# Optimization experiments

Measured on AMD Instinct MI355X. Metric: run time of the kernel, lower is better.

The kernel has to match this reference:

```python
import jax, jax.numpy as jnp
import numpy as np

EPS = 1e-5
N_HEAD = 8
D_MODEL = 1024
D_K = D_MODEL // N_HEAD


def setup_inputs() -> dict:
    key = jax.random.key(0)
    ks = jax.random.split(key, 6)
    B, N = 4, 8192
    scale = 0.02
    return {
        "query": jax.random.normal(ks[0], (B, N, D_MODEL), jnp.float32),
        "key": jax.random.normal(ks[1], (B, N, D_MODEL), jnp.float32),
        "value": jax.random.normal(ks[2], (B, N, D_MODEL), jnp.float32),
        "Wq": jax.random.normal(ks[3], (D_MODEL, D_MODEL), jnp.float32) * scale,
        "bq": jnp.zeros((D_MODEL,), jnp.float32),
        "Wk": jax.random.normal(ks[4], (D_MODEL, D_MODEL), jnp.float32) * scale,
        "bk": jnp.zeros((D_MODEL,), jnp.float32),
        "Wv": jax.random.normal(ks[5], (D_MODEL, D_MODEL), jnp.float32) * scale,
        "bv": jnp.zeros((D_MODEL,), jnp.float32),
        "gamma_K": jnp.ones((N_HEAD, D_K), jnp.float32),
        "beta_K": jnp.zeros((N_HEAD, D_K), jnp.float32),
        "gamma_V": jnp.ones((N_HEAD, D_K), jnp.float32),
        "beta_V": jnp.zeros((N_HEAD, D_K), jnp.float32),
    }


def _proj_heads(x, W, b):
    # x: [B,N,D], torch Linear: x @ W.T + b -> [B,H,N,d_k]
    B, N, _ = x.shape
    y = jnp.einsum('bnd,ed->bne', x, W) + b
    return y.reshape(B, N, N_HEAD, D_K).transpose(0, 2, 1, 3)


def _layernorm_per_head(x, gamma, beta):
    # x: [B,H,N,d_k]; gamma/beta: [H,d_k] broadcast over batch and seq
    mu = jnp.mean(x, axis=-1, keepdims=True)
    var = jnp.mean((x - mu) ** 2, axis=-1, keepdims=True)
    xn = (x - mu) * jax.lax.rsqrt(var + EPS)
    return xn * gamma[None, :, None, :] + beta[None, :, None, :]


def reference(query, key, value, Wq, bq, Wk, bk, Wv, bv,
              gamma_K, beta_K, gamma_V, beta_V):
    B, N, _ = query.shape
    q = _proj_heads(query, Wq, bq)   # [B,H,N,dk]
    k = _proj_heads(key, Wk, bk)
    v = _proj_heads(value, Wv, bv)
    # galerkin: layernorm on K and V per head
    k = _layernorm_per_head(k, gamma_K, beta_K)
    v = _layernorm_per_head(v, gamma_V, beta_V)
    # linear attention: (K^T V)/N then Q @ (.)
    scores = jnp.einsum('bhnd,bhne->bhde', k, v)  # [B,H,dk,dk]
    p_attn = scores / N
    x = jnp.einsum('bhnd,bhde->bhne', q, p_attn)  # [B,H,N,dk]
    att_output = x.transpose(0, 2, 1, 3).reshape(B, N, N_HEAD * D_K)
    return (att_output, p_attn)
```

## Files before the change

kernel.cpp:

```cpp
#include <hip/hip_runtime.h>
#include <stdint.h>

#define DM 1024
#define NHEAD 8
#define DK 128
#define BATCH 4
#define SEQ 8192
#define ROWS (BATCH*SEQ)
#define EPSL 1e-5f
#define NSPLIT 8

typedef __attribute__((ext_vector_type(8)))  short    bf16x8;
typedef __attribute__((ext_vector_type(4)))  short    short4v;
typedef __attribute__((ext_vector_type(4)))  float    f32x4;
typedef __attribute__((ext_vector_type(4)))  float    float4v;
typedef __attribute__((ext_vector_type(2)))  uint32_t uint2v;
typedef __attribute__((ext_vector_type(4)))  uint32_t uint4v;

union AFrag { bf16x8 v; short4v h[2]; int i4[4]; };
union U8    { uint4v v[2]; uint32_t u[8]; };

__device__ inline uint32_t pack2bf(float a, float b){
  uint32_t ua = __builtin_bit_cast(uint32_t, a) + 0x8000u;
  uint32_t ub = __builtin_bit_cast(uint32_t, b) + 0x8000u;
  return (ua >> 16) | (ub & 0xffff0000u);
}

__global__ void wconv_kernel(const float* __restrict__ src, uint32_t* __restrict__ dst, int n8){
  int i = blockIdx.x*256 + threadIdx.x;
  if (i >= n8) return;
  const float4v* s = (const float4v*)src;
  float4v v0 = s[2*i], v1 = s[2*i+1];
  uint4v o;
  o.x = pack2bf(v0.x, v0.y); o.y = pack2bf(v0.z, v0.w);
  o.z = pack2bf(v1.x, v1.y); o.w = pack2bf(v1.z, v1.w);
  ((uint4v*)dst)[i] = o;
}

template<int MODE>
__global__ __launch_bounds__(256, 2)
void gemm_core(const float* __restrict__ A, const uint16_t* __restrict__ Bw,
               const float* __restrict__ bias, const float* __restrict__ gamma,
               const float* __restrict__ beta, uint16_t* __restrict__ outb,
               float* __restrict__ outf)
{
  __shared__ uint16_t As[128][36];
  __shared__ uint16_t Bs[128][36];
  __shared__ float red_s[2][128];
  __shared__ float red_q[2][128];

  const int tid = threadIdx.x;
  const int bN = blockIdx.x, bM = blockIdx.y;
  const int lane = tid & 63, wv = tid >> 6;
  const int wm = wv & 1, wn = wv >> 1;
  const int l15 = lane & 15, l4 = lane >> 4;

  const int sr = tid >> 1, sh = tid & 1;
  const float* Ap = A + (size_t)(bM*128 + sr)*DM + sh*16;
  const uint16_t* Bbase = Bw + (MODE==1 ? (size_t)(bM>>6)*1048576 : (size_t)0);
  const uint16_t* Bp = Bbase + (size_t)(bN*128 + sr)*DM + sh*16;
  uint32_t* asw = (uint32_t*)&As[sr][sh*16];
  uint32_t* bsw = (uint32_t*)&Bs[sr][sh*16];

  f32x4 acc[4][4];
  #pragma unroll
  for (int i=0;i<4;i++)
    #pragma unroll
    for (int j=0;j<4;j++) acc[i][j] = (f32x4)(0.0f);

  const uint16_t* Ard = &As[wm*64 + l15][l4*8];
  const uint16_t* Brd = &Bs[wn*64 + l15][l4*8];

  for (int k0 = 0; k0 < DM; k0 += 32){
    float4v a0 = *(const float4v*)(Ap);
    float4v a1 = *(const float4v*)(Ap+4);
    float4v a2 = *(const float4v*)(Ap+8);
    float4v a3 = *(const float4v*)(Ap+12);
    uint4v b0 = *(const uint4v*)(Bp);
    uint4v b1 = *(const uint4v*)(Bp+8);
    Ap += 32; Bp += 32;
    uint32_t p0 = pack2bf(a0.x,a0.y), p1 = pack2bf(a0.z,a0.w);
    uint32_t p2 = pack2bf(a1.x,a1.y), p3 = pack2bf(a1.z,a1.w);
    uint32_t p4 = pack2bf(a2.x,a2.y), p5 = pack2bf(a2.z,a2.w);
    uint32_t p6 = pack2bf(a3.x,a3.y), p7 = pack2bf(a3.z,a3.w);
    __syncthreads();
    { uint2v t; t.x=p0;   t.y=p1;   ((uint2v*)asw)[0]=t; }
    { uint2v t; t.x=p2;   t.y=p3;   ((uint2v*)asw)[1]=t; }
    { uint2v t; t.x=p4;   t.y=p5;   ((uint2v*)asw)[2]=t; }
    { uint2v t; t.x=p6;   t.y=p7;   ((uint2v*)asw)[3]=t; }
    { uint2v t; t.x=b0.x; t.y=b0.y; ((uint2v*)bsw)[0]=t; }
    { uint2v t; t.x=b0.z; t.y=b0.w; ((uint2v*)bsw)[1]=t; }
    { uint2v t; t.x=b1.x; t.y=b1.y; ((uint2v*)bsw)[2]=t; }
    { uint2v t; t.x=b1.z; t.y=b1.w; ((uint2v*)bsw)[3]=t; }
    __syncthreads();

    AFrag af[4], bf4[4];
    #pragma unroll
    for (int mt=0; mt<4; mt++){
      af[mt].h[0] = *(const short4v*)(Ard + mt*16*36);
      af[mt].h[1] = *(const short4v*)(Ard + mt*16*36 + 4);
    }
    #pragma unroll
    for (int nt=0; nt<4; nt++){
      bf4[nt].h[0] = *(const short4v*)(Brd + nt*16*36);
      bf4[nt].h[1] = *(const short4v*)(Brd + nt*16*36 + 4);
    }
    #pragma unroll
    for (int mt=0; mt<4; mt++)
      #pragma unroll
      for (int nt=0; nt<4; nt++)
        acc[mt][nt] = __builtin_amdgcn_mfma_f32_16x16x32_bf16(af[mt].v, bf4[nt].v, acc[mt][nt], 0, 0, 0);
  }

  if (MODE == 0){
    float bv[4], gv[4], btv[4];
    #pragma unroll
    for (int nt=0; nt<4; nt++){
      int col = bN*128 + wn*64 + nt*16 + l15;
      bv[nt] = bias[col]; gv[nt] = gamma[col]; btv[nt] = beta[col];
    }
    #pragma unroll
    for (int mt=0; mt<4; mt++){
      #pragma unroll
      for (int i=0; i<4; i++){
        float sm = 0.f, sq = 0.f;
        #pragma unroll
        for (int nt=0; nt<4; nt++){
          float v = acc[mt][nt][i] + bv[nt];
          acc[mt][nt][i] = v;
          sm += v; sq += v*v;
        }
        #pragma unroll
        for (int off=1; off<16; off<<=1){
          sm += __shfl_xor(sm, off, 16);
          sq += __shfl_xor(sq, off, 16);
        }
        if (l15 == 0){
          int rl = wm*64 + mt*16 + l4*4 + i;
          red_s[wn][rl] = sm; red_q[wn][rl] = sq;
        }
      }
    }
    __syncthreads();
    #pragma unroll
    for (int mt=0; mt<4; mt++){
      #pragma unroll
      for (int i=0; i<4; i++){
        int rl = wm*64 + mt*16 + l4*4 + i;
        float sum = red_s[0][rl] + red_s[1][rl];
        float ssq = red_q[0][rl] + red_q[1][rl];
        float mean = sum * (1.f/DK);
        float var  = ssq * (1.f/DK) - mean*mean;
        float rs   = rsqrtf(var + EPSL);
        size_t row = (size_t)(bM*128 + rl);
        #pragma unroll
        for (int nt=0; nt<4; nt++){
          int col = bN*128 + wn*64 + nt*16 + l15;
          float o = (acc[mt][nt][i] - mean)*rs*gv[nt] + btv[nt];
          uint32_t u = __builtin_bit_cast(uint32_t, o) + 0x8000u;
          outb[row*DM + col] = (uint16_t)(u >> 16);
        }
      }
    }
  } else {
    const int bb = bM >> 6;
    float bv[4];
    #pragma unroll
    for (int nt=0; nt<4; nt++)
      bv[nt] = bias[bb*DM + bN*128 + wn*64 + nt*16 + l15];
    #pragma unroll
    for (int mt=0; mt<4; mt++){
      #pragma unroll
      for (int i=0; i<4; i++){
        size_t row = (size_t)(bM*128 + wm*64 + mt*16 + l4*4 + i);
        #pragma unroll
        for (int nt=0; nt<4; nt++){
          int col = bN*128 + wn*64 + nt*16 + l15;
          outf[row*DM + col] = acc[mt][nt][i] + bv[nt];
        }
      }
    }
  }
}

__global__ __launch_bounds__(256, 2)
void scores_kernel(const uint16_t* __restrict__ kln, const uint16_t* __restrict__ vln,
                   float* __restrict__ part)
{
  __shared__ uint16_t kT[128][70];
  __shared__ uint16_t vT[128][70];
  const int tid = threadIdx.x;
  const int sp = blockIdx.x & 7, bh = blockIdx.x >> 3;
  const int b = bh >> 3, h = bh & 7;
  const int lane = tid & 63, wv = tid >> 6, wm = wv & 1, wn = wv >> 1;
  const int l15 = lane & 15, l4 = lane >> 4;
  const int dg = tid & 7, np = tid >> 3;

  f32x4 acc[4][4];
  #pragma unroll
  for (int i=0;i<4;i++)
    #pragma unroll
    for (int j=0;j<4;j++) acc[i][j] = (f32x4)(0.0f);

  const size_t hb = (size_t)b*SEQ*DM + (size_t)h*DK;
  for (int nc = 0; nc < 16; nc++){
    const int n0 = sp*1024 + nc*64;
    const uint16_t* kp = kln + hb + (size_t)(n0 + 2*np)*DM + dg*16;
    const uint16_t* vp = vln + hb + (size_t)(n0 + 2*np)*DM + dg*16;
    U8 k0, k1, v0, v1;
    k0.v[0] = *(const uint4v*)(kp);       k0.v[1] = *(const uint4v*)(kp+8);
    k1.v[0] = *(const uint4v*)(kp+DM);    k1.v[1] = *(const uint4v*)(kp+DM+8);
    v0.v[0] = *(const uint4v*)(vp);       v0.v[1] = *(const uint4v*)(vp+8);
    v1.v[0] = *(const uint4v*)(vp+DM);    v1.v[1] = *(const uint4v*)(vp+DM+8);
    __syncthreads();
    #pragma unroll
    for (int q=0; q<8; q++){
      uint32_t ke = (k0.u[q] & 0xffffu) | (k1.u[q] << 16);
      uint32_t ko = (k0.u[q] >> 16)     | (k1.u[q] & 0xffff0000u);
      uint32_t ve = (v0.u[q] & 0xffffu) | (v1.u[q] << 16);
      uint32_t vo = (v0.u[q] >> 16)     | (v1.u[q] & 0xffff0000u);
      int d = dg*16 + q*2;
      *(uint32_t*)&kT[d  ][2*np] = ke;
      *(uint32_t*)&kT[d+1][2*np] = ko;
      *(uint32_t*)&vT[d  ][2*np] = ve;
      *(uint32_t*)&vT[d+1][2*np] = vo;
    }
    __syncthreads();
    #pragma unroll
    for (int ks=0; ks<2; ks++){
      const int koff = ks*32 + l4*8;
      AFrag af[4], bf4[4];
      #pragma unroll
      for (int mt=0; mt<4; mt++){
        const uint16_t* pr = &kT[wm*64 + mt*16 + l15][koff];
        af[mt].i4[0] = *(const int*)(pr);
        af[mt].i4[1] = *(const int*)(pr+2);
        af[mt].i4[2] = *(const int*)(pr+4);
        af[mt].i4[3] = *(const int*)(pr+6);
      }
      #pragma unroll
      for (int nt=0; nt<4; nt++){
        const uint16_t* pr = &vT[wn*64 + nt*16 + l15][koff];
        bf4[nt].i4[0] = *(const int*)(pr);
        bf4[nt].i4[1] = *(const int*)(pr+2);
        bf4[nt].i4[2] = *(const int*)(pr+4);
        bf4[nt].i4[3] = *(const int*)(pr+6);
      }
      #pragma unroll
      for (int mt=0; mt<4; mt++)
        #pragma unroll
        for (int nt=0; nt<4; nt++)
          acc[mt][nt] = __builtin_amdgcn_mfma_f32_16x16x32_bf16(af[mt].v, bf4[nt].v, acc[mt][nt], 0, 0, 0);
    }
  }
  float* po = part + (size_t)(sp*32 + bh)*16384;
  #pragma unroll
  for (int mt=0; mt<4; mt++)
    #pragma unroll
    for (int i=0; i<4; i++){
      int d = wm*64 + mt*16 + l4*4 + i;
      #pragma unroll
      for (int nt=0; nt<4; nt++){
        int e = wn*64 + nt*16 + l15;
        po[d*128 + e] = acc[mt][nt][i];
      }
    }
}

__global__ void reduce_kernel(const float* __restrict__ part, float* __restrict__ pout){
  int i = blockIdx.x*256 + threadIdx.x;
  const float4v* p4 = (const float4v*)part;
  float4v s = p4[i];
  #pragma unroll
  for (int sp2=1; sp2<NSPLIT; sp2++) s += p4[(size_t)sp2*131072 + i];
  s *= (1.0f/(float)SEQ);
  ((float4v*)pout)[i] = s;
}

__global__ __launch_bounds__(256)
void fold_kernel(const float* __restrict__ Wq, const float* __restrict__ p,
                 uint16_t* __restrict__ WcT)
{
  const int dblk = blockIdx.x, h = blockIdx.y, b = blockIdx.z;
  const int t = threadIdx.x;
  const int eg = t & 15, dq = t >> 4;
  const int e0 = eg*8, d0 = dq*8;
  const float* pbase = p + (size_t)((b*NHEAD + h)*DK)*DK;
  const float* wbase = Wq + (size_t)h*DK*DM + dblk*128;
  float accf[8][8];
  #pragma unroll
  for (int i=0;i<8;i++)
    #pragma unroll
    for (int j=0;j<8;j++) accf[i][j] = 0.f;
  for (int f=0; f<DK; f++){
    float4v pa = *(const float4v*)(pbase + f*DK + e0);
    float4v pc = *(const float4v*)(pbase + f*DK + e0 + 4);
    float4v wa = *(const float4v*)(wbase + (size_t)f*DM + d0);
    float4v wc = *(const float4v*)(wbase + (size_t)f*DM + d0 + 4);
    float pe[8] = {pa.x,pa.y,pa.z,pa.w,pc.x,pc.y,pc.z,pc.w};
    float we[8] = {wa.x,wa.y,wa.z,wa.w,wc.x,wc.y,wc.z,wc.w};
    #pragma unroll
    for (int i=0;i<8;i++)
      #pragma unroll
      for (int j=0;j<8;j++) accf[i][j] += pe[i]*we[j];
  }
  uint16_t* ob = WcT + (size_t)b*1048576 + (size_t)(h*DK)*DM + dblk*128;
  #pragma unroll
  for (int i=0;i<8;i++){
    uint4v ov;
    ov.x = pack2bf(accf[i][0], accf[i][1]);
    ov.y = pack2bf(accf[i][2], accf[i][3]);
    ov.z = pack2bf(accf[i][4], accf[i][5]);
    ov.w = pack2bf(accf[i][6], accf[i][7]);
    *(uint4v*)(ob + (size_t)(e0+i)*DM + d0) = ov;
  }
}

__global__ void bc_kernel(const float* __restrict__ bq, const float* __restrict__ p,
                          float* __restrict__ bc)
{
  int gid = blockIdx.x*256 + threadIdx.x;
  int b = gid >> 10, col = gid & 1023, h = col >> 7, e = col & 127;
  float s = 0.f;
  for (int f=0; f<DK; f++)
    s += bq[h*DK + f] * p[(size_t)((b*NHEAD + h)*DK + f)*DK + e];
  bc[gid] = s;
}

extern "C" void kernel_launch(void* const* d_in, const int* in_sizes, int n_in,
                              void* d_out, int out_size, void* d_ws, size_t ws_size,
                              hipStream_t stream)
{
  const float* query = (const float*)d_in[0];
  const float* key   = (const float*)d_in[1];
  const float* value = (const float*)d_in[2];
  const float* Wq    = (const float*)d_in[3];
  const float* bq    = (const float*)d_in[4];
  const float* Wk    = (const float*)d_in[5];
  const float* bk    = (const float*)d_in[6];
  const float* Wv    = (const float*)d_in[7];
  const float* bv    = (const float*)d_in[8];
  const float* gK    = (const float*)d_in[9];
  const float* bK    = (const float*)d_in[10];
  const float* gV    = (const float*)d_in[11];
  const float* bV    = (const float*)d_in[12];
  float* out = (float*)d_out;

  char* ws = (char*)d_ws;
  uint16_t* kln  = (uint16_t*)(ws);
  uint16_t* vln  = (uint16_t*)(ws + 67108864);
  uint16_t* wkb  = (uint16_t*)(ws + 134217728);
  uint16_t* wvb  = (uint16_t*)(ws + 136314880);
  float*    part = (float*)   (ws + 138412032);
  uint16_t* wct  = (uint16_t*)(ws + 155189248);
  float*    bc   = (float*)   (ws + 163577856);

  float* pout = out + 33554432;

  wconv_kernel<<<512, 256, 0, stream>>>(Wk, (uint32_t*)wkb, 131072);
  wconv_kernel<<<512, 256, 0, stream>>>(Wv, (uint32_t*)wvb, 131072);
  gemm_core<0><<<dim3(8,256), 256, 0, stream>>>(key,   wkb, bk, gK, bK, kln, nullptr);
  gemm_core<0><<<dim3(8,256), 256, 0, stream>>>(value, wvb, bv, gV, bV, vln, nullptr);
  scores_kernel<<<256, 256, 0, stream>>>(kln, vln, part);
  reduce_kernel<<<512, 256, 0, stream>>>(part, pout);
  fold_kernel<<<dim3(8,8,4), 256, 0, stream>>>(Wq, pout, wct);
  bc_kernel<<<16, 256, 0, stream>>>(bq, pout, bc);
  gemm_core<1><<<dim3(8,256), 256, 0, stream>>>(query, wct, bc, nullptr, nullptr, nullptr, out);
}
```

Baseline: 924.2 us.

## Prefetch next K-slab into registers and remap GEMM blocks across XCDs

The GEMM and scores kernels now issue the global loads for the next K (or sequence) slab right after the LDS write barrier, so memory latency overlaps the MFMA work on the current slab. The GEMM grid becomes 1D with an XCD-aware mapping: the 8 N-tiles of one M-row land on the same XCD, which is meant to improve L2 reuse of the A rows. The prefetch keeps more registers live, which could pressure occupancy under launch_bounds(256,2).

```diff
diff --git a/kernel.cpp b/kernel.cpp
--- a/kernel.cpp
+++ b/kernel.cpp
@@ -50,7 +50,10 @@
   __shared__ float red_q[2][128];
 
   const int tid = threadIdx.x;
-  const int bN = blockIdx.x, bM = blockIdx.y;
+  const int id  = blockIdx.x;
+  const int xcd = id & 7, j = id >> 3;
+  const int bM  = ((j >> 3) << 3) | xcd;
+  const int bN  = j & 7;
   const int lane = tid & 63, wv = tid >> 6;
   const int wm = wv & 1, wn = wv >> 1;
   const int l15 = lane & 15, l4 = lane >> 4;
@@ -66,33 +69,45 @@
   #pragma unroll
   for (int i=0;i<4;i++)
     #pragma unroll
-    for (int j=0;j<4;j++) acc[i][j] = (f32x4)(0.0f);
+    for (int jj=0;jj<4;jj++) acc[i][jj] = (f32x4)(0.0f);
 
   const uint16_t* Ard = &As[wm*64 + l15][l4*8];
   const uint16_t* Brd = &Bs[wn*64 + l15][l4*8];
 
+  float4v a0 = *(const float4v*)(Ap);
+  float4v a1 = *(const float4v*)(Ap+4);
+  float4v a2 = *(const float4v*)(Ap+8);
+  float4v a3 = *(const float4v*)(Ap+12);
+  uint4v  b0 = *(const uint4v*)(Bp);
+  uint4v  b1 = *(const uint4v*)(Bp+8);
+  Ap += 32; Bp += 32;
+
   for (int k0 = 0; k0 < DM; k0 += 32){
-    float4v a0 = *(const float4v*)(Ap);
-    float4v a1 = *(const float4v*)(Ap+4);
-    float4v a2 = *(const float4v*)(Ap+8);
-    float4v a3 = *(const float4v*)(Ap+12);
-    uint4v b0 = *(const uint4v*)(Bp);
-    uint4v b1 = *(const uint4v*)(Bp+8);
-    Ap += 32; Bp += 32;
     uint32_t p0 = pack2bf(a0.x,a0.y), p1 = pack2bf(a0.z,a0.w);
     uint32_t p2 = pack2bf(a1.x,a1.y), p3 = pack2bf(a1.z,a1.w);
     uint32_t p4 = pack2bf(a2.x,a2.y), p5 = pack2bf(a2.z,a2.w);
     uint32_t p6 = pack2bf(a3.x,a3.y), p7 = pack2bf(a3.z,a3.w);
+    uint4v  c0 = b0, c1 = b1;
     __syncthreads();
     { uint2v t; t.x=p0;   t.y=p1;   ((uint2v*)asw)[0]=t; }
     { uint2v t; t.x=p2;   t.y=p3;   ((uint2v*)asw)[1]=t; }
     { uint2v t; t.x=p4;   t.y=p5;   ((uint2v*)asw)[2]=t; }
     { uint2v t; t.x=p6;   t.y=p7;   ((uint2v*)asw)[3]=t; }
-    { uint2v t; t.x=b0.x; t.y=b0.y; ((uint2v*)bsw)[0]=t; }
-    { uint2v t; t.x=b0.z; t.y=b0.w; ((uint2v*)bsw)[1]=t; }
-    { uint2v t; t.x=b1.x; t.y=b1.y; ((uint2v*)bsw)[2]=t; }
-    { uint2v t; t.x=b1.z; t.y=b1.w; ((uint2v*)bsw)[3]=t; }
-    __syncthreads();
+    { uint2v t; t.x=c0.x; t.y=c0.y; ((uint2v*)bsw)[0]=t; }
+    { uint2v t; t.x=c0.z; t.y=c0.w; ((uint2v*)bsw)[1]=t; }
+    { uint2v t; t.x=c1.x; t.y=c1.y; ((uint2v*)bsw)[2]=t; }
+    { uint2v t; t.x=c1.z; t.y=c1.w; ((uint2v*)bsw)[3]=t; }
+    __syncthreads();
+
+    if (k0 + 32 < DM){
+      a0 = *(const float4v*)(Ap);
+      a1 = *(const float4v*)(Ap+4);
+      a2 = *(const float4v*)(Ap+8);
+      a3 = *(const float4v*)(Ap+12);
+      b0 = *(const uint4v*)(Bp);
+      b1 = *(const uint4v*)(Bp+8);
+      Ap += 32; Bp += 32;
+    }
 
     AFrag af[4], bf4[4];
     #pragma unroll
@@ -200,18 +215,24 @@
   #pragma unroll
   for (int i=0;i<4;i++)
     #pragma unroll
-    for (int j=0;j<4;j++) acc[i][j] = (f32x4)(0.0f);
+    for (int jj=0;jj<4;jj++) acc[i][jj] = (f32x4)(0.0f);
 
   const size_t hb = (size_t)b*SEQ*DM + (size_t)h*DK;
-  for (int nc = 0; nc < 16; nc++){
+
+  auto load_slab = [&](int nc, U8& k0, U8& k1, U8& v0, U8& v1){
     const int n0 = sp*1024 + nc*64;
     const uint16_t* kp = kln + hb + (size_t)(n0 + 2*np)*DM + dg*16;
     const uint16_t* vp = vln + hb + (size_t)(n0 + 2*np)*DM + dg*16;
-    U8 k0, k1, v0, v1;
     k0.v[0] = *(const uint4v*)(kp);       k0.v[1] = *(const uint4v*)(kp+8);
     k1.v[0] = *(const uint4v*)(kp+DM);    k1.v[1] = *(const uint4v*)(kp+DM+8);
     v0.v[0] = *(const uint4v*)(vp);       v0.v[1] = *(const uint4v*)(vp+8);
     v1.v[0] = *(const uint4v*)(vp+DM);    v1.v[1] = *(const uint4v*)(vp+DM+8);
+  };
+
+  U8 k0, k1, v0, v1;
+  load_slab(0, k0, k1, v0, v1);
+
+  for (int nc = 0; nc < 16; nc++){
     __syncthreads();
     #pragma unroll
     for (int q=0; q<8; q++){
@@ -226,6 +247,9 @@
       *(uint32_t*)&vT[d+1][2*np] = vo;
     }
     __syncthreads();
+
+    if (nc + 1 < 16) load_slab(nc + 1, k0, k1, v0, v1);
+
     #pragma unroll
     for (int ks=0; ks<2; ks++){
       const int koff = ks*32 + l4*8;
@@ -291,7 +315,7 @@
   #pragma unroll
   for (int i=0;i<8;i++)
     #pragma unroll
-    for (int j=0;j<8;j++) accf[i][j] = 0.f;
+    for (int jj=0;jj<8;jj++) accf[i][jj] = 0.f;
   for (int f=0; f<DK; f++){
     float4v pa = *(const float4v*)(pbase + f*DK + e0);
     float4v pc = *(const float4v*)(pbase + f*DK + e0 + 4);
@@ -302,7 +326,7 @@
     #pragma unroll
     for (int i=0;i<8;i++)
       #pragma unroll
-      for (int j=0;j<8;j++) accf[i][j] += pe[i]*we[j];
+      for (int jj=0;jj<8;jj++) accf[i][jj] += pe[i]*we[jj];
   }
   uint16_t* ob = WcT + (size_t)b*1048576 + (size_t)(h*DK)*DM + dblk*128;
   #pragma unroll
@@ -359,11 +383,11 @@
 
   wconv_kernel<<<512, 256, 0, stream>>>(Wk, (uint32_t*)wkb, 131072);
   wconv_kernel<<<512, 256, 0, stream>>>(Wv, (uint32_t*)wvb, 131072);
-  gemm_core<0><<<dim3(8,256), 256, 0, stream>>>(key,   wkb, bk, gK, bK, kln, nullptr);
-  gemm_core<0><<<dim3(8,256), 256, 0, stream>>>(value, wvb, bv, gV, bV, vln, nullptr);
+  gemm_core<0><<<2048, 256, 0, stream>>>(key,   wkb, bk, gK, bK, kln, nullptr);
+  gemm_core<0><<<2048, 256, 0, stream>>>(value, wvb, bv, gV, bV, vln, nullptr);
   scores_kernel<<<256, 256, 0, stream>>>(kln, vln, part);
   reduce_kernel<<<512, 256, 0, stream>>>(part, pout);
   fold_kernel<<<dim3(8,8,4), 256, 0, stream>>>(Wq, pout, wct);
   bc_kernel<<<16, 256, 0, stream>>>(bq, pout, bc);
-  gemm_core<1><<<dim3(8,256), 256, 0, stream>>>(query, wct, bc, nullptr, nullptr, nullptr, out);
-}
+  gemm_core<1><<<2048, 256, 0, stream>>>(query, wct, bc, nullptr, nullptr, nullptr, out);
+}
```

Measured after the change: 879.0 us. 4.9% less time.
